# Kernel tuning notes

Measured on AMD Instinct MI355X. Metric: run time of the kernel, lower is better.

Reference implementation:

```python
import jax, jax.numpy as jnp
import numpy as np
from jax import lax

N, D = 4096, 256
MAX_ITERS = 10
SHIFT_THRESHOLD = 1e-5
EPS = 1e-8


def _cosine_sim(a, b):
    # rows of a (M,D) vs rows of b (N,D) -> (M,N)
    an = a / jnp.clip(jnp.linalg.norm(a, axis=-1, keepdims=True), EPS)
    bn = b / jnp.clip(jnp.linalg.norm(b, axis=-1, keepdims=True), EPS)
    return an @ bn.T


def _mean_shift(x, sigma):
    inv_gamma = 1.0 / (2.0 * sigma ** 2)

    def step(carry, _):
        centroids, done = carry
        sim = _cosine_sim(centroids, x)                 # (N, N)
        weights = jnp.exp(2.0 * (sim - 1.0) * inv_gamma)
        new_c = (weights @ x) / jnp.sum(weights, axis=-1, keepdims=True)
        shift = jnp.max(jnp.linalg.norm(new_c - centroids, axis=-1))
        below = shift < SHIFT_THRESHOLD
        # torch breaks BEFORE assigning, so if below threshold keep old centroids
        centroids = jnp.where(done | below, centroids, new_c)
        return (centroids, done | below), None

    (centroids, _), _ = lax.scan(step, (x, jnp.array(False)), None, length=MAX_ITERS)
    return centroids


def _nms_mask(x, centroids, bandwidth):
    # Returns a boolean keep mask over the N centroids (jit-friendly analogue of
    # returning the unique kept indices).
    cp_dist = 2.0 * (1.0 - _cosine_sim(centroids, x))   # (M, N)
    p_to_closest_c = jnp.argmin(cp_dist, axis=0)        # (N,) closest centroid per point
    counts = jnp.zeros((centroids.shape[0],), dtype=jnp.float32).at[p_to_closest_c].add(1.0)
    cc_dist = 2.0 * (1.0 - _cosine_sim(centroids, centroids))
    cc_close = (cc_dist < bandwidth).astype(jnp.float32)
    # For every centroid row: index of the close centroid with the largest count.
    mapped = jnp.argmax(cc_close * counts[None, :], axis=1)   # (M,)
    valid = counts > 0                                        # rows in torch's closest_c
    keep = jnp.zeros((centroids.shape[0],), dtype=bool).at[mapped].max(valid)
    return keep


def setup_inputs() -> dict:
    key = jax.random.key(0)
    x = jax.random.normal(key, (N, D), dtype=jnp.float32)
    sigma = jnp.array(1.0, dtype=jnp.float32)
    return {"x": x, "sigma": sigma}


def reference(x, sigma):
    centroids = _mean_shift(x, sigma)
    keep = _nms_mask(x, centroids, sigma)
    # torch returns centroids[keep_idx] (data-dependent shape); for a jit-friendly
    # reference we return the full centroids plus the keep mask.
    return centroids, keep
```

## Files before the change

### kernel.cpp

```cpp
#include <hip/hip_runtime.h>
#include <math.h>

#define NPTS 4096
#define DIM  256
#define MAX_ITERS 10
#define EPSN 1e-8f
#define NSPL 16

typedef __bf16 bf16x8 __attribute__((ext_vector_type(8)));
typedef float  f32x4  __attribute__((ext_vector_type(4)));
typedef unsigned short u16x8 __attribute__((ext_vector_type(8)));
typedef unsigned short u16x4 __attribute__((ext_vector_type(4)));
typedef unsigned short U16;

__device__ __forceinline__ U16 bf16_rne(float f) {
    unsigned int u = __float_as_uint(f);
    u += 0x7FFFu + ((u >> 16) & 1u);
    return (U16)(u >> 16);
}

__device__ __forceinline__ void glds16(const void* g, void* l) {
    __builtin_amdgcn_global_load_lds(
        (const __attribute__((address_space(1))) unsigned int*)g,
        (__attribute__((address_space(3))) unsigned int*)l,
        16, 0, 0);
}

__global__ void initK(int* counts, int* keep, int* done, int* shiftb, int* acc) {
    int i = blockIdx.x * 256 + threadIdx.x;
    if (i < NPTS) { counts[i] = 0; keep[i] = 0; }
    if (i == 0) { *done = 0; *shiftb = 0; *acc = 0; }
}

__global__ void normxK(const float* __restrict__ x, float* __restrict__ c0,
                       U16* __restrict__ xh, U16* __restrict__ xl) {
    int m = blockIdx.x, t = threadIdx.x;
    float v = x[(size_t)m*DIM + t];
    __shared__ float red[256];
    red[t] = v*v; __syncthreads();
    for (int s = 128; s > 0; s >>= 1) { if (t < s) red[t] += red[t+s]; __syncthreads(); }
    float rn = 1.0f / fmaxf(sqrtf(red[0]), EPSN);
    float hv = v*rn;
    U16 hb = bf16_rne(hv);
    float hf = __uint_as_float((unsigned)hb << 16);
    U16 lb = bf16_rne(hv - hf);
    c0[(size_t)m*DIM + t] = v;
    xh[(size_t)m*DIM + t] = hb;
    xl[(size_t)m*DIM + t] = lb;
}

__global__ void transpK(const float* __restrict__ x, U16* __restrict__ Xth, U16* __restrict__ Xtl) {
    int bm = blockIdx.x, bd = blockIdx.y;
    int t = threadIdx.x;
    __shared__ float sh[32][33];
    int r = t >> 3, cq = (t & 7) * 4;
    float4 v = *(const float4*)&x[(size_t)(bm*32 + r)*DIM + bd*32 + cq];
    sh[r][cq] = v.x; sh[r][cq+1] = v.y; sh[r][cq+2] = v.z; sh[r][cq+3] = v.w;
    __syncthreads();
    int dd = t >> 3, mq = (t & 7) * 4;
    u16x4 h4, l4;
    #pragma unroll
    for (int j = 0; j < 4; ++j) {
        float f = sh[mq + j][dd];
        U16 hb = bf16_rne(f);
        h4[j] = hb;
        l4[j] = bf16_rne(f - __uint_as_float((unsigned)hb << 16));
    }
    size_t off = (size_t)(bd*32 + dd)*NPTS + bm*32 + mq;
    *(u16x4*)&Xth[off] = h4;
    *(u16x4*)&Xtl[off] = l4;
}

#define WPAD 136
__global__ __launch_bounds__(256, 1) void fusedK(
    const U16* __restrict__ chh, const U16* __restrict__ chl,
    const U16* __restrict__ xh,  const U16* __restrict__ xl,
    const U16* __restrict__ xth, const U16* __restrict__ xtl,
    float* __restrict__ cnum, float* __restrict__ psum,
    const int* __restrict__ done, const float* __restrict__ sigma,
    int KLEN)
{
    if (*done) return;
    const int tid  = threadIdx.x;
    const int lane = tid & 63, wq = tid >> 6;
    const int l15  = lane & 15, lg = lane >> 4;
    const int slice = blockIdx.x;
    const int mblk  = blockIdx.y * 64;
    const int j0g  = slice * KLEN;

    __shared__ U16 WhL[64 * WPAD];
    __shared__ U16 WlL[64 * WPAD];
    __shared__ float psw[4][64];

    const float ig = 1.0f / (2.0f * (*sigma) * (*sigma));

    f32x4 acc2[4][4];
    #pragma unroll
    for (int a = 0; a < 4; ++a)
        #pragma unroll
        for (int b = 0; b < 4; ++b) { f32x4 z = {0.f,0.f,0.f,0.f}; acc2[a][b] = z; }
    float rs[4][4];
    #pragma unroll
    for (int a = 0; a < 4; ++a)
        #pragma unroll
        for (int i = 0; i < 4; ++i) rs[a][i] = 0.f;

    const int NJT = KLEN / 128;
    for (int jt = 0; jt < NJT; ++jt) {
        const int jb = j0g + jt * 128;

        f32x4 acc1[4][2];
        #pragma unroll
        for (int a = 0; a < 4; ++a)
            #pragma unroll
            for (int b = 0; b < 2; ++b) { f32x4 z = {0.f,0.f,0.f,0.f}; acc1[a][b] = z; }

        #pragma unroll
        for (int ks = 0; ks < 8; ++ks) {
            const int k0 = ks * 32 + lg * 8;
            bf16x8 ah[4], al[4], bh[2], bl[2];
            #pragma unroll
            for (int a = 0; a < 4; ++a) {
                size_t off = (size_t)(mblk + a*16 + l15)*DIM + k0;
                ah[a] = *(const bf16x8*)(chh + off);
                al[a] = *(const bf16x8*)(chl + off);
            }
            #pragma unroll
            for (int b = 0; b < 2; ++b) {
                size_t off = (size_t)(jb + wq*32 + b*16 + l15)*DIM + k0;
                bh[b] = *(const bf16x8*)(xh + off);
                bl[b] = *(const bf16x8*)(xl + off);
            }
            #pragma unroll
            for (int a = 0; a < 4; ++a)
                #pragma unroll
                for (int b = 0; b < 2; ++b) {
                    acc1[a][b] = __builtin_amdgcn_mfma_f32_16x16x32_bf16(ah[a], bh[b], acc1[a][b], 0,0,0);
                    acc1[a][b] = __builtin_amdgcn_mfma_f32_16x16x32_bf16(ah[a], bl[b], acc1[a][b], 0,0,0);
                    acc1[a][b] = __builtin_amdgcn_mfma_f32_16x16x32_bf16(al[a], bh[b], acc1[a][b], 0,0,0);
                }
        }

        __syncthreads();
        #pragma unroll
        for (int a = 0; a < 4; ++a)
            #pragma unroll
            for (int b = 0; b < 2; ++b)
                #pragma unroll
                for (int i = 0; i < 4; ++i) {
                    float w = __expf(2.0f * (acc1[a][b][i] - 1.0f) * ig);
                    U16 hb = bf16_rne(w);
                    float hf = __uint_as_float((unsigned)hb << 16);
                    U16 lb = bf16_rne(w - hf);
                    int m = a*16 + lg*4 + i;
                    int j = wq*32 + b*16 + l15;
                    WhL[m*WPAD + j] = hb;
                    WlL[m*WPAD + j] = lb;
                    rs[a][i] += w;
                }
        __syncthreads();

        #pragma unroll
        for (int ks = 0; ks < 4; ++ks) {
            bf16x8 wh[4], wl[4], xbh[4], xbl[4];
            const int jl = ks*32 + lg*8;
            #pragma unroll
            for (int a = 0; a < 4; ++a) {
                int m = a*16 + l15;
                wh[a] = *(const bf16x8*)&WhL[m*WPAD + jl];
                wl[a] = *(const bf16x8*)&WlL[m*WPAD + jl];
            }
            #pragma unroll
            for (int b = 0; b < 4; ++b) {
                size_t off = (size_t)(wq*64 + b*16 + l15)*NPTS + jb + jl;
                xbh[b] = *(const bf16x8*)(xth + off);
                xbl[b] = *(const bf16x8*)(xtl + off);
            }
            #pragma unroll
            for (int a = 0; a < 4; ++a)
                #pragma unroll
                for (int b = 0; b < 4; ++b) {
                    acc2[a][b] = __builtin_amdgcn_mfma_f32_16x16x32_bf16(wh[a], xbh[b], acc2[a][b], 0,0,0);
                    acc2[a][b] = __builtin_amdgcn_mfma_f32_16x16x32_bf16(wh[a], xbl[b], acc2[a][b], 0,0,0);
                    acc2[a][b] = __builtin_amdgcn_mfma_f32_16x16x32_bf16(wl[a], xbh[b], acc2[a][b], 0,0,0);
                }
        }
    }

    #pragma unroll
    for (int msk = 1; msk < 16; msk <<= 1)
        #pragma unroll
        for (int a = 0; a < 4; ++a)
            #pragma unroll
            for (int i = 0; i < 4; ++i)
                rs[a][i] += __shfl_xor(rs[a][i], msk, 64);
    if (l15 == 0) {
        #pragma unroll
        for (int a = 0; a < 4; ++a)
            #pragma unroll
            for (int i = 0; i < 4; ++i)
                psw[wq][a*16 + lg*4 + i] = rs[a][i];
    }
    __syncthreads();
    if (tid < 64)
        psum[(size_t)slice*NPTS + mblk + tid] =
            psw[0][tid] + psw[1][tid] + psw[2][tid] + psw[3][tid];

    #pragma unroll
    for (int a = 0; a < 4; ++a)
        #pragma unroll
        for (int b = 0; b < 4; ++b)
            #pragma unroll
            for (int i = 0; i < 4; ++i) {
                int m = mblk + a*16 + lg*4 + i;
                int d = wq*64 + b*16 + l15;
                cnum[((size_t)slice*NPTS + m)*DIM + d] = acc2[a][b][i];
            }
}

__global__ void reduceK(const float* __restrict__ psum, const float* __restrict__ cnum,
                        const float* __restrict__ cprev, float* __restrict__ ccur,
                        U16* __restrict__ chh, U16* __restrict__ chl,
                        const int* __restrict__ done, int* __restrict__ shiftb, int spl)
{
    if (*done) return;
    int m = blockIdx.x, t = threadIdx.x;
    float rowsum = 0.f;
    for (int s = 0; s < spl; ++s) rowsum += psum[(size_t)s*NPTS + m];
    float num = 0.f;
    for (int s = 0; s < spl; ++s) num += cnum[((size_t)s*NPTS + m)*DIM + t];
    float cn = num / rowsum;
    ccur[(size_t)m*DIM + t] = cn;
    float d = cn - cprev[(size_t)m*DIM + t];
    __shared__ float redd[256], redn[256];
    redd[t] = d*d; redn[t] = cn*cn;
    __syncthreads();
    for (int st = 128; st > 0; st >>= 1) {
        if (t < st) { redd[t] += redd[t+st]; redn[t] += redn[t+st]; }
        __syncthreads();
    }
    if (t == 0) atomicMax(shiftb, __float_as_int(sqrtf(redd[0])));
    float rn = 1.0f / fmaxf(sqrtf(redn[0]), EPSN);
    float hv = cn * rn;
    U16 hb = bf16_rne(hv);
    float hf = __uint_as_float((unsigned)hb << 16);
    U16 lb = bf16_rne(hv - hf);
    chh[(size_t)m*DIM + t] = hb;
    chl[(size_t)m*DIM + t] = lb;
}

__global__ void flagK(int* done, int* shiftb, int* acc, int curidx) {
    if (!*done) {
        float sh = __int_as_float(*shiftb);
        if (sh < 1e-5f) *done = 1;
        else *acc = curidx;
    }
    *shiftb = 0;
}

__global__ void finalK(const float* __restrict__ p0, const float* __restrict__ p1,
                       const float* __restrict__ p2, const int* __restrict__ acc,
                       float* __restrict__ out) {
    int i = blockIdx.x*256 + threadIdx.x;
    const float* p = (*acc == 0) ? p0 : ((*acc == 1) ? p1 : p2);
    out[i] = p[i];
}

__global__ void normfinalK(const float* __restrict__ p0, const float* __restrict__ p1,
                           const float* __restrict__ p2, const int* __restrict__ acc,
                           U16* __restrict__ hh, U16* __restrict__ ll) {
    int m = blockIdx.x, t = threadIdx.x;
    const float* p = (*acc == 0) ? p0 : ((*acc == 1) ? p1 : p2);
    float v = p[(size_t)m*DIM + t];
    __shared__ float red[256];
    red[t] = v*v; __syncthreads();
    for (int s = 128; s > 0; s >>= 1) { if (t < s) red[t] += red[t+s]; __syncthreads(); }
    float rn = 1.0f / fmaxf(sqrtf(red[0]), EPSN);
    float hv = v*rn;
    U16 hb = bf16_rne(hv);
    float hf = __uint_as_float((unsigned)hb << 16);
    U16 lb = bf16_rne(hv - hf);
    hh[(size_t)m*DIM + t] = hb;
    ll[(size_t)m*DIM + t] = lb;
}

__global__ __launch_bounds__(256) void argminMK(
    const U16* __restrict__ Ph, const U16* __restrict__ Pl,
    const U16* __restrict__ Ch, const U16* __restrict__ Cl,
    float* __restrict__ aval, int* __restrict__ aidx)
{
    const int tid = threadIdx.x;
    const int lane = tid & 63, wid = tid >> 6;
    const int wr = wid & 1, wc = wid >> 1;
    const int P  = blockIdx.x * 128;
    const int ms = blockIdx.y;
    const int M0 = ms * (NPTS / NSPL);

    __shared__ U16 S[4][4096];
    __shared__ float fmv[128][2];
    __shared__ int   fmi[128][2];

    float pv[16];
    int   pm[16];
    #pragma unroll
    for (int s = 0; s < 16; ++s) { pv[s] = 3.4e38f; pm[s] = 0; }

    for (int mt = 0; mt < (NPTS/NSPL)/128; ++mt) {
        const int M = M0 + mt*128;
        f32x4 acc[4][4];
        #pragma unroll
        for (int a = 0; a < 4; ++a)
            #pragma unroll
            for (int b = 0; b < 4; ++b) { f32x4 z = {0.f,0.f,0.f,0.f}; acc[a][b] = z; }

        for (int k0 = 0; k0 < DIM; k0 += 32) {
            __syncthreads();
            #pragma unroll
            for (int h = 0; h < 2; ++h) {
                const int sb   = wid * 128 + h * 64;
                const int slot = sb + lane;
                const int row  = slot & 127, kg = slot >> 7;
                const int col  = k0 + kg * 8;
                glds16(Ph + (size_t)(P + row)*DIM + col, &S[0][(size_t)sb * 8]);
                glds16(Pl + (size_t)(P + row)*DIM + col, &S[1][(size_t)sb * 8]);
                glds16(Ch + (size_t)(M + row)*DIM + col, &S[2][(size_t)sb * 8]);
                glds16(Cl + (size_t)(M + row)*DIM + col, &S[3][(size_t)sb * 8]);
            }
            __syncthreads();
            bf16x8 fah[4], fal[4], fbh[4], fbl[4];
            const int roff = (lane >> 4) * 128 + (lane & 15);
            #pragma unroll
            for (int f = 0; f < 4; ++f) {
                const int sA = roff + wr*64 + f*16;
                const int sB = roff + wc*64 + f*16;
                fah[f] = *(const bf16x8*)&S[0][(size_t)sA * 8];
                fal[f] = *(const bf16x8*)&S[1][(size_t)sA * 8];
                fbh[f] = *(const bf16x8*)&S[2][(size_t)sB * 8];
                fbl[f] = *(const bf16x8*)&S[3][(size_t)sB * 8];
            }
            #pragma unroll
            for (int a = 0; a < 4; ++a)
                #pragma unroll
                for (int b = 0; b < 4; ++b) {
                    acc[a][b] = __builtin_amdgcn_mfma_f32_16x16x32_bf16(fah[a], fbh[b], acc[a][b], 0,0,0);
                    acc[a][b] = __builtin_amdgcn_mfma_f32_16x16x32_bf16(fah[a], fbl[b], acc[a][b], 0,0,0);
                    acc[a][b] = __builtin_amdgcn_mfma_f32_16x16x32_bf16(fal[a], fbh[b], acc[a][b], 0,0,0);
                }
        }
        #pragma unroll
        for (int a = 0; a < 4; ++a)
            #pragma unroll
            for (int i = 0; i < 4; ++i) {
                const int s = a*4 + i;
                #pragma unroll
                for (int b = 0; b < 4; ++b) {
                    float d = 2.0f*(1.0f - acc[a][b][i]);
                    int m = M + wc*64 + b*16 + (lane & 15);
                    if (d < pv[s] || (d == pv[s] && m < pm[s])) { pv[s]=d; pm[s]=m; }
                }
            }
    }
    #pragma unroll
    for (int msk = 1; msk < 16; msk <<= 1)
        #pragma unroll
        for (int s = 0; s < 16; ++s) {
            float v2 = __shfl_xor(pv[s], msk, 64);
            int   m2 = __shfl_xor(pm[s], msk, 64);
            if (v2 < pv[s] || (v2 == pv[s] && m2 < pm[s])) { pv[s]=v2; pm[s]=m2; }
        }
    if ((lane & 15) == 0) {
        #pragma unroll
        for (int a = 0; a < 4; ++a)
            #pragma unroll
            for (int i = 0; i < 4; ++i) {
                int row = wr*64 + a*16 + (lane>>4)*4 + i;
                fmv[row][wc] = pv[a*4+i];
                fmi[row][wc] = pm[a*4+i];
            }
    }
    __syncthreads();
    if (tid < 128) {
        float v = fmv[tid][0]; int m = fmi[tid][0];
        float v1 = fmv[tid][1]; int m1 = fmi[tid][1];
        if (v1 < v || (v1 == v && m1 < m)) { v=v1; m=m1; }
        aval[(size_t)ms*NPTS + P + tid] = v;
        aidx[(size_t)ms*NPTS + P + tid] = m;
    }
}

__global__ void acombineK(const float* __restrict__ aval, const int* __restrict__ aidx,
                          int* __restrict__ counts)
{
    int p = blockIdx.x*256 + threadIdx.x;
    float bv = 3.4e38f; int bm = 1<<30;
    for (int s = 0; s < NSPL; ++s) {
        float v = aval[(size_t)s*NPTS + p]; int m = aidx[(size_t)s*NPTS + p];
        if (v < bv || (v == bv && m < bm)) { bv=v; bm=m; }
    }
    atomicAdd(&counts[bm], 1);
}

__global__ __launch_bounds__(256) void ccMK(
    const U16* __restrict__ Ch, const U16* __restrict__ Cl,
    const int* __restrict__ counts, const float* __restrict__ sigma,
    float* __restrict__ cval, int* __restrict__ cidx)
{
    const int tid = threadIdx.x;
    const int lane = tid & 63, wid = tid >> 6;
    const int wr = wid & 1, wc = wid >> 1;
    const int Mrow = blockIdx.x * 128;
    const int js   = blockIdx.y;
    const int J0   = js * (NPTS / NSPL);
    const float bw = *sigma;

    __shared__ U16 S[4][4096];
    __shared__ float gmv[128][2];
    __shared__ int   gmi[128][2];
    __shared__ float scnt[128];

    float mvv[16];
    int   mjj[16];
    #pragma unroll
    for (int s = 0; s < 16; ++s) { mvv[s] = -1.f; mjj[s] = 1<<30; }

    for (int jt = 0; jt < (NPTS/NSPL)/128; ++jt) {
        const int J = J0 + jt*128;
        __syncthreads();
        if (tid < 128) scnt[tid] = (float)counts[J + tid];
        f32x4 acc[4][4];
        #pragma unroll
        for (int a = 0; a < 4; ++a)
            #pragma unroll
            for (int b = 0; b < 4; ++b) { f32x4 z = {0.f,0.f,0.f,0.f}; acc[a][b] = z; }

        for (int k0 = 0; k0 < DIM; k0 += 32) {
            __syncthreads();
            #pragma unroll
            for (int h = 0; h < 2; ++h) {
                const int sb   = wid * 128 + h * 64;
                const int slot = sb + lane;
                const int row  = slot & 127, kg = slot >> 7;
                const int col  = k0 + kg * 8;
                glds16(Ch + (size_t)(Mrow + row)*DIM + col, &S[0][(size_t)sb * 8]);
                glds16(Cl + (size_t)(Mrow + row)*DIM + col, &S[1][(size_t)sb * 8]);
                glds16(Ch + (size_t)(J + row)*DIM + col,    &S[2][(size_t)sb * 8]);
                glds16(Cl + (size_t)(J + row)*DIM + col,    &S[3][(size_t)sb * 8]);
            }
            __syncthreads();
            bf16x8 fah[4], fal[4], fbh[4], fbl[4];
            const int roff = (lane >> 4) * 128 + (lane & 15);
            #pragma unroll
            for (int f = 0; f < 4; ++f) {
                const int sA = roff + wr*64 + f*16;
                const int sB = roff + wc*64 + f*16;
                fah[f] = *(const bf16x8*)&S[0][(size_t)sA * 8];
                fal[f] = *(const bf16x8*)&S[1][(size_t)sA * 8];
                fbh[f] = *(const bf16x8*)&S[2][(size_t)sB * 8];
                fbl[f] = *(const bf16x8*)&S[3][(size_t)sB * 8];
            }
            #pragma unroll
            for (int a = 0; a < 4; ++a)
                #pragma unroll
                for (int b = 0; b < 4; ++b) {
                    acc[a][b] = __builtin_amdgcn_mfma_f32_16x16x32_bf16(fah[a], fbh[b], acc[a][b], 0,0,0);
                    acc[a][b] = __builtin_amdgcn_mfma_f32_16x16x32_bf16(fah[a], fbl[b], acc[a][b], 0,0,0);
                    acc[a][b] = __builtin_amdgcn_mfma_f32_16x16x32_bf16(fal[a], fbh[b], acc[a][b], 0,0,0);
                }
        }
        #pragma unroll
        for (int a = 0; a < 4; ++a)
            #pragma unroll
            for (int i = 0; i < 4; ++i) {
                const int s = a*4 + i;
                #pragma unroll
                for (int b = 0; b < 4; ++b) {
                    float d = 2.0f*(1.0f - acc[a][b][i]);
                    int jl = wc*64 + b*16 + (lane & 15);
                    float val = (d < bw) ? scnt[jl] : 0.0f;
                    int j = J + jl;
                    if (val > mvv[s] || (val == mvv[s] && j < mjj[s])) { mvv[s]=val; mjj[s]=j; }
                }
            }
    }
    #pragma unroll
    for (int msk = 1; msk < 16; msk <<= 1)
        #pragma unroll
        for (int s = 0; s < 16; ++s) {
            float v2 = __shfl_xor(mvv[s], msk, 64);
            int   j2 = __shfl_xor(mjj[s], msk, 64);
            if (v2 > mvv[s] || (v2 == mvv[s] && j2 < mjj[s])) { mvv[s]=v2; mjj[s]=j2; }
        }
    if ((lane & 15) == 0) {
        #pragma unroll
        for (int a = 0; a < 4; ++a)
            #pragma unroll
            for (int i = 0; i < 4; ++i) {
                int row = wr*64 + a*16 + (lane>>4)*4 + i;
                gmv[row][wc] = mvv[a*4+i];
                gmi[row][wc] = mjj[a*4+i];
            }
    }
    __syncthreads();
    if (tid < 128) {
        float v = gmv[tid][0]; int j = gmi[tid][0];
        float v1 = gmv[tid][1]; int j1 = gmi[tid][1];
        if (v1 > v || (v1 == v && j1 < j)) { v=v1; j=j1; }
        cval[(size_t)js*NPTS + Mrow + tid] = v;
        cidx[(size_t)js*NPTS + Mrow + tid] = j;
    }
}

__global__ void ccombineK(const float* __restrict__ cval, const int* __restrict__ cidx,
                          const int* __restrict__ counts, int* __restrict__ keep)
{
    int m = blockIdx.x*256 + threadIdx.x;
    float bv = -1.0f; int bj = 1<<30;
    for (int s = 0; s < NSPL; ++s) {
        float v = cval[(size_t)s*NPTS + m]; int j = cidx[(size_t)s*NPTS + m];
        if (v > bv || (v == bv && j < bj)) { bv=v; bj=j; }
    }
    if (counts[m] > 0) atomicOr(&keep[bj], 1);
}

__global__ void keepwriteK(const int* __restrict__ keep, float* __restrict__ out)
{
    int i = blockIdx.x*256 + threadIdx.x;
    out[(size_t)NPTS*DIM + i] = keep[i] ? 1.0f : 0.0f;
}

extern "C" void kernel_launch(void* const* d_in, const int* in_sizes, int n_in,
                              void* d_out, int out_size, void* d_ws, size_t ws_size,
                              hipStream_t stream)
{
    const float* x     = (const float*)d_in[0];
    const float* sigma = (const float*)d_in[1];
    float* out = (float*)d_out;

    const size_t ND4 = (size_t)NPTS * DIM * 4;
    const size_t NDu = (size_t)NPTS * DIM * 2;

    const int spls[] = {8, 4, 2};
    int SPL = 2;
    size_t o_xh=0,o_xl=0,o_xth=0,o_xtl=0,o_chh=0,o_chl=0,o_c0=0,o_c1=0,o_c2=0,
           o_cnum=0,o_psum=0,o_aval=0,o_aidx=0,o_cval=0,o_cidx=0,
           o_counts=0,o_keep=0,o_done=0,o_shift=0,o_acc=0;

    for (int ci = 0; ci < 3; ++ci) {
        int spl = spls[ci];
        size_t off = 0;
        auto take = [&](size_t nb) { size_t a = off; off += (nb + 255) & ~(size_t)255; return a; };
        o_xh  = take(NDu);  o_xl  = take(NDu);
        o_xth = take(NDu);  o_xtl = take(NDu);
        o_chh = take(NDu);  o_chl = take(NDu);
        o_c0  = take(ND4);  o_c1  = take(ND4);  o_c2 = take(ND4);
        o_cnum = take((size_t)spl * ND4);
        o_psum = take((size_t)spl * NPTS * 4);
        o_aval = take((size_t)NSPL*NPTS*4); o_aidx = take((size_t)NSPL*NPTS*4);
        o_cval = take((size_t)NSPL*NPTS*4); o_cidx = take((size_t)NSPL*NPTS*4);
        o_counts = take((size_t)NPTS*4);    o_keep = take((size_t)NPTS*4);
        o_done = take(256); o_shift = take(256); o_acc = take(256);
        SPL = spl;
        if (off <= ws_size) break;
    }
    const int KLEN = NPTS / SPL;

    char* W = (char*)d_ws;
    U16* xh  = (U16*)(W + o_xh);   U16* xl  = (U16*)(W + o_xl);
    U16* xth = (U16*)(W + o_xth);  U16* xtl = (U16*)(W + o_xtl);
    U16* chh = (U16*)(W + o_chh);  U16* chl = (U16*)(W + o_chl);
    float* cb[3] = { (float*)(W + o_c0), (float*)(W + o_c1), (float*)(W + o_c2) };
    float* cnum = (float*)(W + o_cnum);
    float* psum = (float*)(W + o_psum);
    float* aval = (float*)(W + o_aval); int* aidx = (int*)(W + o_aidx);
    float* cval = (float*)(W + o_cval); int* cidx = (int*)(W + o_cidx);
    int* counts = (int*)(W + o_counts); int* keep = (int*)(W + o_keep);
    int* done   = (int*)(W + o_done);   int* shiftb = (int*)(W + o_shift);
    int* acc    = (int*)(W + o_acc);

    initK  <<<dim3(16), dim3(256), 0, stream>>>(counts, keep, done, shiftb, acc);
    normxK <<<dim3(NPTS), dim3(256), 0, stream>>>(x, cb[0], xh, xl);
    transpK<<<dim3(128, 8), dim3(256), 0, stream>>>(x, xth, xtl);

    for (int it = 0; it < MAX_ITERS; ++it) {
        const U16* ah = (it == 0) ? xh : chh;
        const U16* al = (it == 0) ? xl : chl;
        const int cur = 1 + (it & 1);
        const int prv = (it == 0) ? 0 : 1 + ((it - 1) & 1);
        fusedK<<<dim3(SPL, NPTS/64), dim3(256), 0, stream>>>(
            ah, al, xh, xl, xth, xtl, cnum, psum, done, sigma, KLEN);
        reduceK<<<dim3(NPTS), dim3(256), 0, stream>>>(
            psum, cnum, cb[prv], cb[cur], chh, chl, done, shiftb, SPL);
        flagK<<<dim3(1), dim3(1), 0, stream>>>(done, shiftb, acc, cur);
    }

    finalK    <<<dim3(NPTS), dim3(256), 0, stream>>>(cb[0], cb[1], cb[2], acc, out);
    normfinalK<<<dim3(NPTS), dim3(256), 0, stream>>>(cb[0], cb[1], cb[2], acc, chh, chl);

    argminMK<<<dim3(NPTS/128, NSPL), dim3(256), 0, stream>>>(xh, xl, chh, chl, aval, aidx);
    acombineK<<<dim3(NPTS/256), dim3(256), 0, stream>>>(aval, aidx, counts);
    ccMK    <<<dim3(NPTS/128, NSPL), dim3(256), 0, stream>>>(chh, chl, counts, sigma, cval, cidx);
    ccombineK<<<dim3(NPTS/256), dim3(256), 0, stream>>>(cval, cidx, counts, keep);
    keepwriteK<<<dim3(NPTS/256), dim3(256), 0, stream>>>(keep, out);
}
```

Before: 1.765 ms.

## Use 8 waves per fused mean-shift block and shrink split-K factors

Moves the fused similarity/weight/accumulate kernel from 4 waves of 256 threads to 8 waves of 512 threads, halving each wave's tile in both GEMM stages (16 columns in the first, 32 output dims in the second). The split-K candidates also drop from {8,4,2} to {4,2,1}, so fewer partial numerators are written to and reduced from global memory. The aim is more latency hiding and lower register pressure per wave, plus less reduction traffic. The cost is fewer blocks, which may leave CUs underfilled, and smaller per-wave MFMA tiles that reuse each loaded operand less.

Result: slower. 2.351 ms (+33.2%).

```diff
diff --git a/kernel.cpp b/kernel.cpp
--- a/kernel.cpp
+++ b/kernel.cpp
@@ -72,7 +72,7 @@
 }
 
 #define WPAD 136
-__global__ __launch_bounds__(256, 1) void fusedK(
+__global__ __launch_bounds__(512, 2) void fusedK(
     const U16* __restrict__ chh, const U16* __restrict__ chl,
     const U16* __restrict__ xh,  const U16* __restrict__ xl,
     const U16* __restrict__ xth, const U16* __restrict__ xtl,
@@ -90,15 +90,15 @@
 
     __shared__ U16 WhL[64 * WPAD];
     __shared__ U16 WlL[64 * WPAD];
-    __shared__ float psw[4][64];
+    __shared__ float psw[8][64];
 
     const float ig = 1.0f / (2.0f * (*sigma) * (*sigma));
 
-    f32x4 acc2[4][4];
+    f32x4 acc2[4][2];
     #pragma unroll
     for (int a = 0; a < 4; ++a)
         #pragma unroll
-        for (int b = 0; b < 4; ++b) { f32x4 z = {0.f,0.f,0.f,0.f}; acc2[a][b] = z; }
+        for (int b = 0; b < 2; ++b) { f32x4 z = {0.f,0.f,0.f,0.f}; acc2[a][b] = z; }
     float rs[4][4];
     #pragma unroll
     for (int a = 0; a < 4; ++a)
@@ -109,60 +109,53 @@
     for (int jt = 0; jt < NJT; ++jt) {
         const int jb = j0g + jt * 128;
 
-        f32x4 acc1[4][2];
-        #pragma unroll
-        for (int a = 0; a < 4; ++a)
-            #pragma unroll
-            for (int b = 0; b < 2; ++b) { f32x4 z = {0.f,0.f,0.f,0.f}; acc1[a][b] = z; }
+        f32x4 acc1[4];
+        #pragma unroll
+        for (int a = 0; a < 4; ++a) { f32x4 z = {0.f,0.f,0.f,0.f}; acc1[a] = z; }
 
         #pragma unroll
         for (int ks = 0; ks < 8; ++ks) {
             const int k0 = ks * 32 + lg * 8;
-            bf16x8 ah[4], al[4], bh[2], bl[2];
+            bf16x8 ah[4], al[4], bh, bl;
             #pragma unroll
             for (int a = 0; a < 4; ++a) {
                 size_t off = (size_t)(mblk + a*16 + l15)*DIM + k0;
                 ah[a] = *(const bf16x8*)(chh + off);
                 al[a] = *(const bf16x8*)(chl + off);
             }
-            #pragma unroll
-            for (int b = 0; b < 2; ++b) {
-                size_t off = (size_t)(jb + wq*32 + b*16 + l15)*DIM + k0;
-                bh[b] = *(const bf16x8*)(xh + off);
-                bl[b] = *(const bf16x8*)(xl + off);
-            }
-            #pragma unroll
-            for (int a = 0; a < 4; ++a)
-                #pragma unroll
-                for (int b = 0; b < 2; ++b) {
-                    acc1[a][b] = __builtin_amdgcn_mfma_f32_16x16x32_bf16(ah[a], bh[b], acc1[a][b], 0,0,0);
-                    acc1[a][b] = __builtin_amdgcn_mfma_f32_16x16x32_bf16(ah[a], bl[b], acc1[a][b], 0,0,0);
-                    acc1[a][b] = __builtin_amdgcn_mfma_f32_16x16x32_bf16(al[a], bh[b], acc1[a][b], 0,0,0);
-                }
+            {
+                size_t off = (size_t)(jb + wq*16 + l15)*DIM + k0;
+                bh = *(const bf16x8*)(xh + off);
+                bl = *(const bf16x8*)(xl + off);
+            }
+            #pragma unroll
+            for (int a = 0; a < 4; ++a) {
+                acc1[a] = __builtin_amdgcn_mfma_f32_16x16x32_bf16(ah[a], bh, acc1[a], 0,0,0);
+                acc1[a] = __builtin_amdgcn_mfma_f32_16x16x32_bf16(ah[a], bl, acc1[a], 0,0,0);
+                acc1[a] = __builtin_amdgcn_mfma_f32_16x16x32_bf16(al[a], bh, acc1[a], 0,0,0);
+            }
         }
 
         __syncthreads();
         #pragma unroll
         for (int a = 0; a < 4; ++a)
             #pragma unroll
-            for (int b = 0; b < 2; ++b)
-                #pragma unroll
-                for (int i = 0; i < 4; ++i) {
-                    float w = __expf(2.0f * (acc1[a][b][i] - 1.0f) * ig);
-                    U16 hb = bf16_rne(w);
-                    float hf = __uint_as_float((unsigned)hb << 16);
-                    U16 lb = bf16_rne(w - hf);
-                    int m = a*16 + lg*4 + i;
-                    int j = wq*32 + b*16 + l15;
-                    WhL[m*WPAD + j] = hb;
-                    WlL[m*WPAD + j] = lb;
-                    rs[a][i] += w;
-                }
+            for (int i = 0; i < 4; ++i) {
+                float w = __expf(2.0f * (acc1[a][i] - 1.0f) * ig);
+                U16 hb = bf16_rne(w);
+                float hf = __uint_as_float((unsigned)hb << 16);
+                U16 lb = bf16_rne(w - hf);
+                int m = a*16 + lg*4 + i;
+                int j = wq*16 + l15;
+                WhL[m*WPAD + j] = hb;
+                WlL[m*WPAD + j] = lb;
+                rs[a][i] += w;
+            }
         __syncthreads();
 
         #pragma unroll
         for (int ks = 0; ks < 4; ++ks) {
-            bf16x8 wh[4], wl[4], xbh[4], xbl[4];
+            bf16x8 wh[4], wl[4], xbh[2], xbl[2];
             const int jl = ks*32 + lg*8;
             #pragma unroll
             for (int a = 0; a < 4; ++a) {
@@ -171,15 +164,15 @@
                 wl[a] = *(const bf16x8*)&WlL[m*WPAD + jl];
             }
             #pragma unroll
-            for (int b = 0; b < 4; ++b) {
-                size_t off = (size_t)(wq*64 + b*16 + l15)*NPTS + jb + jl;
+            for (int b = 0; b < 2; ++b) {
+                size_t off = (size_t)(wq*32 + b*16 + l15)*NPTS + jb + jl;
                 xbh[b] = *(const bf16x8*)(xth + off);
                 xbl[b] = *(const bf16x8*)(xtl + off);
             }
             #pragma unroll
             for (int a = 0; a < 4; ++a)
                 #pragma unroll
-                for (int b = 0; b < 4; ++b) {
+                for (int b = 0; b < 2; ++b) {
                     acc2[a][b] = __builtin_amdgcn_mfma_f32_16x16x32_bf16(wh[a], xbh[b], acc2[a][b], 0,0,0);
                     acc2[a][b] = __builtin_amdgcn_mfma_f32_16x16x32_bf16(wh[a], xbl[b], acc2[a][b], 0,0,0);
                     acc2[a][b] = __builtin_amdgcn_mfma_f32_16x16x32_bf16(wl[a], xbh[b], acc2[a][b], 0,0,0);
@@ -202,18 +195,21 @@
                 psw[wq][a*16 + lg*4 + i] = rs[a][i];
     }
     __syncthreads();
-    if (tid < 64)
-        psum[(size_t)slice*NPTS + mblk + tid] =
-            psw[0][tid] + psw[1][tid] + psw[2][tid] + psw[3][tid];
+    if (tid < 64) {
+        float v = 0.f;
+        #pragma unroll
+        for (int q = 0; q < 8; ++q) v += psw[q][tid];
+        psum[(size_t)slice*NPTS + mblk + tid] = v;
+    }
 
     #pragma unroll
     for (int a = 0; a < 4; ++a)
         #pragma unroll
-        for (int b = 0; b < 4; ++b)
+        for (int b = 0; b < 2; ++b)
             #pragma unroll
             for (int i = 0; i < 4; ++i) {
                 int m = mblk + a*16 + lg*4 + i;
-                int d = wq*64 + b*16 + l15;
+                int d = wq*32 + b*16 + l15;
                 cnum[((size_t)slice*NPTS + m)*DIM + d] = acc2[a][b][i];
             }
 }
@@ -539,8 +535,8 @@
     const size_t ND4 = (size_t)NPTS * DIM * 4;
     const size_t NDu = (size_t)NPTS * DIM * 2;
 
-    const int spls[] = {8, 4, 2};
-    int SPL = 2;
+    const int spls[] = {4, 2, 1};
+    int SPL = 1;
     size_t o_xh=0,o_xl=0,o_xth=0,o_xtl=0,o_chh=0,o_chl=0,o_c0=0,o_c1=0,o_c2=0,
            o_cnum=0,o_psum=0,o_aval=0,o_aidx=0,o_cval=0,o_cidx=0,
            o_counts=0,o_keep=0,o_done=0,o_shift=0,o_acc=0;
@@ -586,7 +582,7 @@
         const U16* al = (it == 0) ? xl : chl;
         const int cur = 1 + (it & 1);
         const int prv = (it == 0) ? 0 : 1 + ((it - 1) & 1);
-        fusedK<<<dim3(SPL, NPTS/64), dim3(256), 0, stream>>>(
+        fusedK<<<dim3(SPL, NPTS/64), dim3(512), 0, stream>>>(
             ah, al, xh, xl, xth, xtl, cnum, psum, done, sigma, KLEN);
         reduceK<<<dim3(NPTS), dim3(256), 0, stream>>>(
             psum, cnum, cb[prv], cb[cur], chh, chl, done, shiftb, SPL);
```
